# Kernel tuning notes

Measured on AMD Instinct MI355X. Metric: run time of the kernel, lower is better.

Reference implementation:

```python
import jax, jax.numpy as jnp
import numpy as np

STRIDE = 15           # cfg.shm.dilation_kernel
PAD = STRIDE // 2
P = 1048576           # cfg.shm.max_n_pixel (static sparse-pixel budget)


def dilate(alpha):
    # mask = (0.01 < alpha < 0.99); then 15x15 max-pool, stride 1, pad 7 (same size)
    m = jnp.logical_and(alpha > 0.01, alpha < 0.99).astype(alpha.dtype)
    return jax.lax.reduce_window(
        m, -jnp.inf, jax.lax.max,
        (1, 1, STRIDE, STRIDE), (1, 1, 1, 1),
        [(0, 0), (0, 0), (PAD, PAD), (PAD, PAD)])


def setup_inputs() -> dict:
    key = jax.random.key(0)
    ks = jax.random.split(key, 8)
    d = 128
    return {
        'image': jax.random.normal(ks[0], (8, 3, 512, 512), jnp.float32),
        'lr_pred': jax.random.uniform(ks[1], (8, 1, 512, 512), jnp.float32),
        'W1': jax.random.normal(ks[2], (4, d), jnp.float32) * 0.5,
        'b1': jnp.zeros((d,), jnp.float32),
        'W2': jax.random.normal(ks[3], (d, d), jnp.float32) * (1.0 / np.sqrt(d)),
        'b2': jnp.zeros((d,), jnp.float32),
        'W3': jax.random.normal(ks[4], (d, 1), jnp.float32) * (1.0 / np.sqrt(d)),
        'b3': jnp.zeros((1,), jnp.float32),
    }


def reference(image, lr_pred, W1, b1, W2, b2, W3, b3):
    B, C, H, W = image.shape
    mask = dilate(lr_pred)                       # [B,1,H,W] dilated uncertainty mask

    # generate_sparse_inputs: cat(img, (lr_pred-0.5)/0.5) channels-last, gather where mask>0
    feat = jnp.concatenate([image, (lr_pred - 0.5) / 0.5], axis=1)  # [B,4,H,W]
    feat = feat.transpose(0, 2, 3, 1).reshape(-1, C + 1)            # [B*H*W, 4]
    mflat = mask.reshape(-1)                                        # [B*H*W]

    (idx,) = jnp.nonzero(mflat > 0, size=P, fill_value=0)           # static-size gather
    count = jnp.sum(mflat > 0)
    valid = (jnp.arange(P) < count).astype(feat.dtype)              # [P]

    # torch's generate_sparse_inputs runs under no_grad -> stop_gradient on gather
    x = jax.lax.stop_gradient(feat[idx])                            # [P,4]

    # stand-in sparse head (shm): per-pixel MLP with sigmoid alpha output
    h = jax.nn.relu(x @ W1 + b1)
    h = jax.nn.relu(h @ W2 + b2)
    pred = jax.nn.sigmoid(h @ W3 + b3)[:, 0]                        # [P]

    # scatter predictions back to dense grid; ungathered masked pixels keep lr_pred
    scattered = jnp.zeros_like(mflat).at[idx].add(pred * valid)
    covered = jnp.zeros_like(mflat).at[idx].add(valid)
    lrf = lr_pred.reshape(-1)
    dense = scattered + (1.0 - covered) * lrf

    # final blend: pred*mask + lr_pred*(1-mask)
    final = dense * mflat + lrf * (1.0 - mflat)
    return final.reshape(B, 1, H, W)
```

## Files before the change

### kernel.cpp

```cpp
#include <hip/hip_runtime.h>
#include <hip/hip_bf16.h>
#include <math.h>

#define BB 8
#define HH 512
#define WW 512
#define NPIX (BB * HH * WW)
#define HWPIX (HH * WW)
#define PBUD 1048576
#define RAD 7
#define NB (NPIX / 256)
#define NMLP (NPIX / 128)

typedef __attribute__((ext_vector_type(4))) float f32x4;
typedef __attribute__((ext_vector_type(8))) short short8;
typedef __attribute__((ext_vector_type(2))) unsigned int u32x2;
typedef __attribute__((ext_vector_type(4))) unsigned int u32x4;

__device__ __forceinline__ unsigned short f2bf(float f) {
    unsigned int u = __float_as_uint(f);
    unsigned int r = (u + 0x7fffu + ((u >> 16) & 1u)) >> 16;
    return (unsigned short)r;
}

__device__ __forceinline__ unsigned int pkbf(float a, float b) {
    __hip_bfloat162 h = __float22bfloat162_rn(make_float2(a, b));
    return *(unsigned int*)&h;
}

__global__ void k_prep(const float* __restrict__ w2, const float* __restrict__ w1,
                       const float* __restrict__ b1,
                       unsigned short* __restrict__ w2f, unsigned short* __restrict__ w1f) {
    int i = blockIdx.x * 256 + threadIdx.x;
    if (i < 16384) {
        int e  = i & 7;
        int l  = (i >> 3) & 63;
        int ks = (i >> 9) & 3;
        int jc = i >> 11;
        int j = jc * 16 + (l & 15);
        int k = ks * 32 + ((l >> 4) & 3) * 8 + e;
        w2f[i] = f2bf(w2[k * 128 + j]);
    } else {
        int i2 = i - 16384;
        int e  = i2 & 7;
        int l  = (i2 >> 3) & 63;
        int fi = i2 >> 9;
        int j = fi * 16 + (l & 15);
        int k = ((l >> 4) & 3) * 8 + e;
        float v = (k < 4) ? w1[k * 128 + j] : ((k == 4) ? b1[j] : 0.0f);
        w1f[i2] = f2bf(v);
    }
}

__global__ void k_rowdil(const float* __restrict__ lr, unsigned char* __restrict__ rowdil) {
    int p = blockIdx.x * 256 + threadIdx.x;
    int w = p & (WW - 1);
    int row0 = p - w;
    int lo = w - RAD; if (lo < 0) lo = 0;
    int hi = w + RAD; if (hi > WW - 1) hi = WW - 1;
    unsigned char any = 0;
    for (int x = lo; x <= hi; ++x) {
        float v = lr[row0 + x];
        any |= (unsigned char)(v > 0.01f && v < 0.99f);
    }
    rowdil[p] = any;
}

__global__ void k_coldil(const unsigned char* __restrict__ rowdil,
                         unsigned char* __restrict__ dm,
                         unsigned char* __restrict__ rankb,
                         int* __restrict__ gsum) {
    int p = blockIdx.x * 256 + threadIdx.x;
    int h = (p >> 9) & (HH - 1);
    int lo = h - RAD; if (lo < 0) lo = 0;
    int hi = h + RAD; if (hi > HH - 1) hi = HH - 1;
    lo -= h; hi -= h;
    unsigned char any = 0;
    for (int d = lo; d <= hi; ++d) any |= rowdil[p + d * WW];
    dm[p] = any;

    unsigned long long bal = __ballot(any != 0);
    __shared__ int wsum[4];
    int lane = threadIdx.x & 63;
    int wid  = threadIdx.x >> 6;
    if (lane == 0) wsum[wid] = __popcll(bal);
    __syncthreads();
    int pre = __popcll(bal & ((1ull << lane) - 1ull));
    int woff = 0;
    for (int i = 0; i < wid; ++i) woff += wsum[i];
    rankb[p] = (unsigned char)(woff + pre);
    if (threadIdx.x == 0) gsum[blockIdx.x] = wsum[0] + wsum[1] + wsum[2] + wsum[3];
}

__global__ void k_scan(const int* __restrict__ gsum, int* __restrict__ goff) {
    __shared__ int tsum[1024];
    int t = threadIdx.x;
    int base = t * 8;
    int v[8];
    int s = 0;
#pragma unroll
    for (int i = 0; i < 8; ++i) { v[i] = gsum[base + i]; s += v[i]; }
    tsum[t] = s;
    __syncthreads();
    for (int off = 1; off < 1024; off <<= 1) {
        int x = tsum[t];
        int y = (t >= off) ? tsum[t - off] : 0;
        __syncthreads();
        tsum[t] = x + y;
        __syncthreads();
    }
    int run = (t == 0) ? 0 : tsum[t - 1];
#pragma unroll
    for (int i = 0; i < 8; ++i) { goff[base + i] = run; run += v[i]; }
}

__global__ __launch_bounds__(256, 3)
void k_mlp(const float* __restrict__ image, const float* __restrict__ lr,
           const unsigned short* __restrict__ w1f, const unsigned short* __restrict__ w2f,
           const float* __restrict__ b2, const float* __restrict__ w3,
           const float* __restrict__ b3,
           const unsigned char* __restrict__ dm, const unsigned char* __restrict__ rankb,
           const int* __restrict__ goff, float* __restrict__ out) {
    __shared__ __align__(16) char lds[43008];
    __shared__ int s_any;
    int g  = blockIdx.x;
    int p0 = g * 128;
    int t  = threadIdx.x;

    if (t == 0) s_any = 0;
    __syncthreads();
    float lrv0 = 0.f;
    if (t < 128) {
        int p = p0 + t;
        lrv0 = lr[p];
        if (dm[p] && (goff[p >> 8] + (int)rankb[p] < PBUD)) s_any = 1;
    }
    __syncthreads();
    if (!s_any) {
        if (t < 128) out[p0 + t] = lrv0;
        return;
    }

    if (t < 128) {
        int p = p0 + t;
        size_t bimg = (size_t)(p >> 18) * 3 * HWPIX + (p & (HWPIX - 1));
        float x0 = image[bimg];
        float x1 = image[bimg + HWPIX];
        float x2 = image[bimg + 2 * HWPIX];
        float x3 = 2.0f * lrv0 - 1.0f;
        char* xr = lds + 32768 + t * 80;
        u32x4 d0 = { pkbf(x0, x1), pkbf(x2, x3), pkbf(1.0f, 0.0f), 0u };
        u32x4 z  = { 0u, 0u, 0u, 0u };
        *(u32x4*)(xr)      = d0;
        *(u32x4*)(xr + 16) = z;
        *(u32x4*)(xr + 32) = z;
        *(u32x4*)(xr + 48) = z;
        *(u32x4*)(xr + 64) = z;
    }

    int w    = t >> 6;
    int l    = t & 63;
    int lr16 = l & 15;
    int lh   = (l >> 4) & 3;

    const short8* wf1 = (const short8*)w1f;
    short8 a1_0 = wf1[(w * 2 + 0) * 64 + l];
    short8 a1_1 = wf1[(w * 2 + 1) * 64 + l];
    __syncthreads();

#pragma unroll
    for (int jc = 0; jc < 8; ++jc) {
        int px = jc * 16 + lr16;
        short8 xb = *(const short8*)(lds + 32768 + px * 80 + lh * 16);
        f32x4 c0 = {0.f, 0.f, 0.f, 0.f};
        f32x4 c1 = {0.f, 0.f, 0.f, 0.f};
        c0 = __builtin_amdgcn_mfma_f32_16x16x32_bf16(a1_0, xb, c0, 0, 0, 0);
        c1 = __builtin_amdgcn_mfma_f32_16x16x32_bf16(a1_1, xb, c1, 0, 0, 0);
        int swz = (px & 15) << 4;
        {
            int j0 = (w * 2 + 0) * 16 + lh * 4;
            u32x2 u = { pkbf(fmaxf(c0[0], 0.f), fmaxf(c0[1], 0.f)),
                        pkbf(fmaxf(c0[2], 0.f), fmaxf(c0[3], 0.f)) };
            *(u32x2*)(lds + (((px << 8) | (j0 << 1)) ^ swz)) = u;
        }
        {
            int j1 = (w * 2 + 1) * 16 + lh * 4;
            u32x2 u = { pkbf(fmaxf(c1[0], 0.f), fmaxf(c1[1], 0.f)),
                        pkbf(fmaxf(c1[2], 0.f), fmaxf(c1[3], 0.f)) };
            *(u32x2*)(lds + (((px << 8) | (j1 << 1)) ^ swz)) = u;
        }
    }
    __syncthreads();

    int rowbase = w * 32;
    short8 af[2][4];
#pragma unroll
    for (int ks = 0; ks < 4; ++ks) {
#pragma unroll
        for (int mt = 0; mt < 2; ++mt) {
            int row = rowbase + mt * 16 + lr16;
            int a = (((row << 8) | (ks << 6) | (lh << 4))) ^ ((row & 15) << 4);
            af[mt][ks] = *(const short8*)(lds + a);
        }
    }

    float b2v[8], w3v[8];
#pragma unroll
    for (int jc = 0; jc < 8; ++jc) {
        int col = jc * 16 + lr16;
        b2v[jc] = b2[col];
        w3v[jc] = w3[col];
    }
    float b3v = b3[0];

    f32x4 acc[2][8];
#pragma unroll
    for (int mt = 0; mt < 2; ++mt)
#pragma unroll
        for (int jc = 0; jc < 8; ++jc)
            acc[mt][jc] = (f32x4){b2v[jc], b2v[jc], b2v[jc], b2v[jc]};

    const short8* wf = (const short8*)w2f;
#pragma unroll
    for (int jc = 0; jc < 8; ++jc) {
        short8 bf[4];
#pragma unroll
        for (int ks = 0; ks < 4; ++ks) bf[ks] = wf[(jc * 4 + ks) * 64 + l];
#pragma unroll
        for (int ks = 0; ks < 4; ++ks) {
            acc[0][jc] = __builtin_amdgcn_mfma_f32_16x16x32_bf16(af[0][ks], bf[ks], acc[0][jc], 0, 0, 0);
            acc[1][jc] = __builtin_amdgcn_mfma_f32_16x16x32_bf16(af[1][ks], bf[ks], acc[1][jc], 0, 0, 0);
        }
    }

#pragma unroll
    for (int mt = 0; mt < 2; ++mt) {
#pragma unroll
        for (int r = 0; r < 4; ++r) {
            int row = rowbase + mt * 16 + lh * 4 + r;
            float part = 0.f;
#pragma unroll
            for (int jc = 0; jc < 8; ++jc)
                part += fmaxf(acc[mt][jc][r], 0.f) * w3v[jc];
            part += __shfl_xor(part, 1);
            part += __shfl_xor(part, 2);
            part += __shfl_xor(part, 4);
            part += __shfl_xor(part, 8);
            if (lr16 == 0) {
                int p = p0 + row;
                float lrv = lr[p];
                bool s = dm[p] && (goff[p >> 8] + (int)rankb[p] < PBUD);
                float logit = b3v + part;
                out[p] = s ? (1.0f / (1.0f + __expf(-logit))) : lrv;
            }
        }
    }
}

extern "C" void kernel_launch(void* const* d_in, const int* in_sizes, int n_in,
                              void* d_out, int out_size, void* d_ws, size_t ws_size,
                              hipStream_t stream) {
    const float* image = (const float*)d_in[0];
    const float* lr    = (const float*)d_in[1];
    const float* w1    = (const float*)d_in[2];
    const float* b1    = (const float*)d_in[3];
    const float* w2    = (const float*)d_in[4];
    const float* b2    = (const float*)d_in[5];
    const float* w3    = (const float*)d_in[6];
    const float* b3    = (const float*)d_in[7];
    float* out = (float*)d_out;

    char* ws = (char*)d_ws;
    unsigned char* rowdil = (unsigned char*)ws;
    unsigned char* dm     = (unsigned char*)(ws + (size_t)NPIX);
    unsigned char* rankb  = (unsigned char*)(ws + 2 * (size_t)NPIX);
    int* gsum             = (int*)(ws + 3 * (size_t)NPIX);
    int* goff             = (int*)(ws + 3 * (size_t)NPIX + NB * 4);
    unsigned short* w2f   = (unsigned short*)(ws + 3 * (size_t)NPIX + 2 * NB * 4);
    unsigned short* w1f   = w2f + 16384;

    k_prep  <<<80, 256, 0, stream>>>(w2, w1, b1, w2f, w1f);
    k_rowdil<<<NPIX / 256, 256, 0, stream>>>(lr, rowdil);
    k_coldil<<<NB, 256, 0, stream>>>(rowdil, dm, rankb, gsum);
    k_scan  <<<1, 1024, 0, stream>>>(gsum, goff);
    k_mlp   <<<NMLP, 256, 0, stream>>>(image, lr, w1f, w2f, b2, w3, b3,
                                       dm, rankb, goff, out);
}
```

Before: 152.3 us.

## Split MLP work over 8 waves by output column with LDS reduction

The MLP kernel moves from 4 waves, each owning 32 pixel rows and all 128 hidden columns, to 8 waves, each owning 16 hidden columns across all 128 pixels. Each wave keeps only its slice of W2 in registers and streams activation fragments from LDS, and per-wave partial logits are reduced through LDS before the sigmoid. The input staging shrinks to 16 bytes per pixel plus a shared zero row, and the early-exit test uses a wave ballot instead of a shared flag. The aim is to cut register pressure and raise occupancy. The cost is more LDS reads (activations are re-read by every wave) and an extra barrier for the final reduction.

```diff
diff --git a/kernel.cpp b/kernel.cpp
--- a/kernel.cpp
+++ b/kernel.cpp
@@ -11,6 +11,11 @@
 #define RAD 7
 #define NB (NPIX / 256)
 #define NMLP (NPIX / 128)
+
+#define XOFF  32768
+#define ZROW  (XOFF + 2048)
+#define FLAG0 (XOFF + 2080)
+#define PART  XOFF
 
 typedef __attribute__((ext_vector_type(4))) float f32x4;
 typedef __attribute__((ext_vector_type(8))) short short8;
@@ -114,146 +119,106 @@
     for (int i = 0; i < 8; ++i) { goff[base + i] = run; run += v[i]; }
 }
 
-__global__ __launch_bounds__(256, 3)
+__global__ __launch_bounds__(512, 6)
 void k_mlp(const float* __restrict__ image, const float* __restrict__ lr,
            const unsigned short* __restrict__ w1f, const unsigned short* __restrict__ w2f,
            const float* __restrict__ b2, const float* __restrict__ w3,
            const float* __restrict__ b3,
            const unsigned char* __restrict__ dm, const unsigned char* __restrict__ rankb,
            const int* __restrict__ goff, float* __restrict__ out) {
-    __shared__ __align__(16) char lds[43008];
-    __shared__ int s_any;
-    int g  = blockIdx.x;
-    int p0 = g * 128;
+    __shared__ __align__(16) char lds[36864];
+    int p0 = blockIdx.x * 128;
     int t  = threadIdx.x;
-
-    if (t == 0) s_any = 0;
-    __syncthreads();
-    float lrv0 = 0.f;
+    int w  = t >> 6;
+    int l  = t & 63;
+    int lr16 = l & 15;
+    int lh   = (l >> 4) & 3;
+
+    const short8* wf1 = (const short8*)w1f;
+    short8 a1 = wf1[w * 64 + l];
+    float b2v = b2[w * 16 + lr16];
+    float w3v = w3[w * 16 + lr16];
+    float b3v = b3[0];
+
+    bool  sel = false;
+    float lrv = 0.f;
     if (t < 128) {
         int p = p0 + t;
-        lrv0 = lr[p];
-        if (dm[p] && (goff[p >> 8] + (int)rankb[p] < PBUD)) s_any = 1;
-    }
-    __syncthreads();
-    if (!s_any) {
-        if (t < 128) out[p0 + t] = lrv0;
-        return;
-    }
-
-    if (t < 128) {
-        int p = p0 + t;
+        lrv = lr[p];
+        sel = dm[p] && (goff[p >> 8] + (int)rankb[p] < PBUD);
         size_t bimg = (size_t)(p >> 18) * 3 * HWPIX + (p & (HWPIX - 1));
         float x0 = image[bimg];
         float x1 = image[bimg + HWPIX];
         float x2 = image[bimg + 2 * HWPIX];
-        float x3 = 2.0f * lrv0 - 1.0f;
-        char* xr = lds + 32768 + t * 80;
+        float x3 = 2.0f * lrv - 1.0f;
         u32x4 d0 = { pkbf(x0, x1), pkbf(x2, x3), pkbf(1.0f, 0.0f), 0u };
-        u32x4 z  = { 0u, 0u, 0u, 0u };
-        *(u32x4*)(xr)      = d0;
-        *(u32x4*)(xr + 16) = z;
-        *(u32x4*)(xr + 32) = z;
-        *(u32x4*)(xr + 48) = z;
-        *(u32x4*)(xr + 64) = z;
-    }
-
-    int w    = t >> 6;
-    int l    = t & 63;
-    int lr16 = l & 15;
-    int lh   = (l >> 4) & 3;
-
-    const short8* wf1 = (const short8*)w1f;
-    short8 a1_0 = wf1[(w * 2 + 0) * 64 + l];
-    short8 a1_1 = wf1[(w * 2 + 1) * 64 + l];
-    __syncthreads();
+        *(u32x4*)(lds + XOFF + t * 16) = d0;
+    }
+    if (t == 128) *(u32x4*)(lds + ZROW) = (u32x4){0u, 0u, 0u, 0u};
+    if (t < 128) {
+        unsigned long long bal = __ballot(sel);
+        if (l == 0) *(int*)(lds + FLAG0 + w * 4) = (bal != 0ull) ? 1 : 0;
+    }
+    __syncthreads();
+    int any = *(const int*)(lds + FLAG0) | *(const int*)(lds + FLAG0 + 4);
+    if (!any) {
+        if (t < 128) out[p0 + t] = lrv;
+        return;
+    }
 
 #pragma unroll
     for (int jc = 0; jc < 8; ++jc) {
         int px = jc * 16 + lr16;
-        short8 xb = *(const short8*)(lds + 32768 + px * 80 + lh * 16);
-        f32x4 c0 = {0.f, 0.f, 0.f, 0.f};
-        f32x4 c1 = {0.f, 0.f, 0.f, 0.f};
-        c0 = __builtin_amdgcn_mfma_f32_16x16x32_bf16(a1_0, xb, c0, 0, 0, 0);
-        c1 = __builtin_amdgcn_mfma_f32_16x16x32_bf16(a1_1, xb, c1, 0, 0, 0);
-        int swz = (px & 15) << 4;
-        {
-            int j0 = (w * 2 + 0) * 16 + lh * 4;
-            u32x2 u = { pkbf(fmaxf(c0[0], 0.f), fmaxf(c0[1], 0.f)),
-                        pkbf(fmaxf(c0[2], 0.f), fmaxf(c0[3], 0.f)) };
-            *(u32x2*)(lds + (((px << 8) | (j0 << 1)) ^ swz)) = u;
+        const char* xaddr = (lh == 0) ? (lds + XOFF + px * 16) : (lds + ZROW);
+        short8 xb = *(const short8*)xaddr;
+        f32x4 c = {0.f, 0.f, 0.f, 0.f};
+        c = __builtin_amdgcn_mfma_f32_16x16x32_bf16(a1, xb, c, 0, 0, 0);
+        int j0 = w * 16 + lh * 4;
+        u32x2 u = { pkbf(fmaxf(c[0], 0.f), fmaxf(c[1], 0.f)),
+                    pkbf(fmaxf(c[2], 0.f), fmaxf(c[3], 0.f)) };
+        *(u32x2*)(lds + (((px << 8) | (j0 << 1)) ^ (lr16 << 4))) = u;
+    }
+
+    const short8* wf2 = (const short8*)w2f;
+    short8 bf[4];
+#pragma unroll
+    for (int ks = 0; ks < 4; ++ks) bf[ks] = wf2[(w * 4 + ks) * 64 + l];
+    __syncthreads();
+
+    f32x4 acc[8];
+#pragma unroll
+    for (int mt = 0; mt < 8; ++mt) acc[mt] = (f32x4){b2v, b2v, b2v, b2v};
+#pragma unroll
+    for (int mt = 0; mt < 8; ++mt) {
+#pragma unroll
+        for (int ks = 0; ks < 4; ++ks) {
+            int row = mt * 16 + lr16;
+            short8 af = *(const short8*)(lds + ((((row << 8) | (ks << 6) | (lh << 4))) ^ (lr16 << 4)));
+            acc[mt] = __builtin_amdgcn_mfma_f32_16x16x32_bf16(af, bf[ks], acc[mt], 0, 0, 0);
         }
-        {
-            int j1 = (w * 2 + 1) * 16 + lh * 4;
-            u32x2 u = { pkbf(fmaxf(c1[0], 0.f), fmaxf(c1[1], 0.f)),
-                        pkbf(fmaxf(c1[2], 0.f), fmaxf(c1[3], 0.f)) };
-            *(u32x2*)(lds + (((px << 8) | (j1 << 1)) ^ swz)) = u;
-        }
-    }
-    __syncthreads();
-
-    int rowbase = w * 32;
-    short8 af[2][4];
-#pragma unroll
-    for (int ks = 0; ks < 4; ++ks) {
-#pragma unroll
-        for (int mt = 0; mt < 2; ++mt) {
-            int row = rowbase + mt * 16 + lr16;
-            int a = (((row << 8) | (ks << 6) | (lh << 4))) ^ ((row & 15) << 4);
-            af[mt][ks] = *(const short8*)(lds + a);
-        }
-    }
-
-    float b2v[8], w3v[8];
-#pragma unroll
-    for (int jc = 0; jc < 8; ++jc) {
-        int col = jc * 16 + lr16;
-        b2v[jc] = b2[col];
-        w3v[jc] = w3[col];
-    }
-    float b3v = b3[0];
-
-    f32x4 acc[2][8];
-#pragma unroll
-    for (int mt = 0; mt < 2; ++mt)
-#pragma unroll
-        for (int jc = 0; jc < 8; ++jc)
-            acc[mt][jc] = (f32x4){b2v[jc], b2v[jc], b2v[jc], b2v[jc]};
-
-    const short8* wf = (const short8*)w2f;
-#pragma unroll
-    for (int jc = 0; jc < 8; ++jc) {
-        short8 bf[4];
-#pragma unroll
-        for (int ks = 0; ks < 4; ++ks) bf[ks] = wf[(jc * 4 + ks) * 64 + l];
-#pragma unroll
-        for (int ks = 0; ks < 4; ++ks) {
-            acc[0][jc] = __builtin_amdgcn_mfma_f32_16x16x32_bf16(af[0][ks], bf[ks], acc[0][jc], 0, 0, 0);
-            acc[1][jc] = __builtin_amdgcn_mfma_f32_16x16x32_bf16(af[1][ks], bf[ks], acc[1][jc], 0, 0, 0);
-        }
-    }
-
-#pragma unroll
-    for (int mt = 0; mt < 2; ++mt) {
+    }
+
+#pragma unroll
+    for (int mt = 0; mt < 8; ++mt) {
 #pragma unroll
         for (int r = 0; r < 4; ++r) {
-            int row = rowbase + mt * 16 + lh * 4 + r;
-            float part = 0.f;
-#pragma unroll
-            for (int jc = 0; jc < 8; ++jc)
-                part += fmaxf(acc[mt][jc][r], 0.f) * w3v[jc];
+            float part = fmaxf(acc[mt][r], 0.f) * w3v;
             part += __shfl_xor(part, 1);
             part += __shfl_xor(part, 2);
             part += __shfl_xor(part, 4);
             part += __shfl_xor(part, 8);
             if (lr16 == 0) {
-                int p = p0 + row;
-                float lrv = lr[p];
-                bool s = dm[p] && (goff[p >> 8] + (int)rankb[p] < PBUD);
-                float logit = b3v + part;
-                out[p] = s ? (1.0f / (1.0f + __expf(-logit))) : lrv;
+                int px = mt * 16 + lh * 4 + r;
+                *(float*)(lds + PART + w * 512 + px * 4) = part;
             }
         }
+    }
+    __syncthreads();
+    if (t < 128) {
+        float s = b3v;
+#pragma unroll
+        for (int ww = 0; ww < 8; ++ww) s += *(const float*)(lds + PART + ww * 512 + t * 4);
+        out[p0 + t] = sel ? (1.0f / (1.0f + __expf(-s))) : lrv;
     }
 }
 
@@ -283,6 +248,6 @@
     k_rowdil<<<NPIX / 256, 256, 0, stream>>>(lr, rowdil);
     k_coldil<<<NB, 256, 0, stream>>>(rowdil, dm, rankb, gsum);
     k_scan  <<<1, 1024, 0, stream>>>(gsum, goff);
-    k_mlp   <<<NMLP, 256, 0, stream>>>(image, lr, w1f, w2f, b2, w3, b3,
+    k_mlp   <<<NMLP, 512, 0, stream>>>(image, lr, w1f, w2f, b2, w3, b3,
                                        dm, rankb, goff, out);
 }
```

Result: slower. 186.6 us (+22.5%).

## Compact MLP layer-1 staging, drop barriers, and raise occupancy to four blocks

Applied to the files above, without the earlier changes.

The input staging rows shrink from 80 to 16 bytes, with a shared zero row serving the padded K lanes. The any-selected check becomes a wavefront ballot written to LDS flags, which removes one barrier. Layer 1 is reorganised so each wave computes all 128 hidden units for its own 32 pixels, so the barrier between layer 1 and layer 2 is gone. LDS use falls and launch bounds go from 3 to 4 blocks per CU. This adds register pressure, since all eight W1 fragments are now held per thread, and it relies on each wave reading back only the rows it wrote itself.

```diff
diff --git a/kernel.cpp b/kernel.cpp
--- a/kernel.cpp
+++ b/kernel.cpp
@@ -11,6 +11,10 @@
 #define RAD 7
 #define NB (NPIX / 256)
 #define NMLP (NPIX / 128)
+
+#define XOFF  32768
+#define ZROW  (XOFF + 2048)
+#define FLAGS (XOFF + 2064)
 
 typedef __attribute__((ext_vector_type(4))) float f32x4;
 typedef __attribute__((ext_vector_type(8))) short short8;
@@ -114,85 +118,68 @@
     for (int i = 0; i < 8; ++i) { goff[base + i] = run; run += v[i]; }
 }
 
-__global__ __launch_bounds__(256, 3)
+__global__ __launch_bounds__(256, 4)
 void k_mlp(const float* __restrict__ image, const float* __restrict__ lr,
            const unsigned short* __restrict__ w1f, const unsigned short* __restrict__ w2f,
            const float* __restrict__ b2, const float* __restrict__ w3,
            const float* __restrict__ b3,
            const unsigned char* __restrict__ dm, const unsigned char* __restrict__ rankb,
            const int* __restrict__ goff, float* __restrict__ out) {
-    __shared__ __align__(16) char lds[43008];
-    __shared__ int s_any;
-    int g  = blockIdx.x;
-    int p0 = g * 128;
+    __shared__ __align__(16) char lds[34944];
+    int p0 = blockIdx.x * 128;
     int t  = threadIdx.x;
-
-    if (t == 0) s_any = 0;
-    __syncthreads();
-    float lrv0 = 0.f;
+    int w    = t >> 6;
+    int l    = t & 63;
+    int lr16 = l & 15;
+    int lh   = l >> 4;
+
+    const short8* wf1 = (const short8*)w1f;
+    short8 a1[8];
+#pragma unroll
+    for (int jt = 0; jt < 8; ++jt) a1[jt] = wf1[jt * 64 + l];
+
+    bool  sel = false;
+    float lrv = 0.f;
     if (t < 128) {
         int p = p0 + t;
-        lrv0 = lr[p];
-        if (dm[p] && (goff[p >> 8] + (int)rankb[p] < PBUD)) s_any = 1;
-    }
-    __syncthreads();
-    if (!s_any) {
-        if (t < 128) out[p0 + t] = lrv0;
-        return;
-    }
-
-    if (t < 128) {
-        int p = p0 + t;
+        lrv = lr[p];
+        sel = dm[p] && (goff[p >> 8] + (int)rankb[p] < PBUD);
         size_t bimg = (size_t)(p >> 18) * 3 * HWPIX + (p & (HWPIX - 1));
         float x0 = image[bimg];
         float x1 = image[bimg + HWPIX];
         float x2 = image[bimg + 2 * HWPIX];
-        float x3 = 2.0f * lrv0 - 1.0f;
-        char* xr = lds + 32768 + t * 80;
+        float x3 = 2.0f * lrv - 1.0f;
         u32x4 d0 = { pkbf(x0, x1), pkbf(x2, x3), pkbf(1.0f, 0.0f), 0u };
-        u32x4 z  = { 0u, 0u, 0u, 0u };
-        *(u32x4*)(xr)      = d0;
-        *(u32x4*)(xr + 16) = z;
-        *(u32x4*)(xr + 32) = z;
-        *(u32x4*)(xr + 48) = z;
-        *(u32x4*)(xr + 64) = z;
-    }
-
-    int w    = t >> 6;
-    int l    = t & 63;
-    int lr16 = l & 15;
-    int lh   = (l >> 4) & 3;
-
-    const short8* wf1 = (const short8*)w1f;
-    short8 a1_0 = wf1[(w * 2 + 0) * 64 + l];
-    short8 a1_1 = wf1[(w * 2 + 1) * 64 + l];
+        *(u32x4*)(lds + XOFF + t * 16) = d0;
+        unsigned long long bal = __ballot(sel);
+        if (l == 0) *(int*)(lds + FLAGS + w * 4) = (bal != 0ull) ? 1 : 0;
+    }
+    if (t == 128) *(u32x4*)(lds + ZROW) = (u32x4){0u, 0u, 0u, 0u};
     __syncthreads();
-
-#pragma unroll
-    for (int jc = 0; jc < 8; ++jc) {
-        int px = jc * 16 + lr16;
-        short8 xb = *(const short8*)(lds + 32768 + px * 80 + lh * 16);
-        f32x4 c0 = {0.f, 0.f, 0.f, 0.f};
-        f32x4 c1 = {0.f, 0.f, 0.f, 0.f};
-        c0 = __builtin_amdgcn_mfma_f32_16x16x32_bf16(a1_0, xb, c0, 0, 0, 0);
-        c1 = __builtin_amdgcn_mfma_f32_16x16x32_bf16(a1_1, xb, c1, 0, 0, 0);
-        int swz = (px & 15) << 4;
-        {
-            int j0 = (w * 2 + 0) * 16 + lh * 4;
-            u32x2 u = { pkbf(fmaxf(c0[0], 0.f), fmaxf(c0[1], 0.f)),
-                        pkbf(fmaxf(c0[2], 0.f), fmaxf(c0[3], 0.f)) };
-            *(u32x2*)(lds + (((px << 8) | (j0 << 1)) ^ swz)) = u;
-        }
-        {
-            int j1 = (w * 2 + 1) * 16 + lh * 4;
-            u32x2 u = { pkbf(fmaxf(c1[0], 0.f), fmaxf(c1[1], 0.f)),
-                        pkbf(fmaxf(c1[2], 0.f), fmaxf(c1[3], 0.f)) };
-            *(u32x2*)(lds + (((px << 8) | (j1 << 1)) ^ swz)) = u;
-        }
-    }
-    __syncthreads();
-
-    int rowbase = w * 32;
+    int any = *(const int*)(lds + FLAGS) | *(const int*)(lds + FLAGS + 4);
+    if (!any) {
+        if (t < 128) out[p0 + t] = lrv;
+        return;
+    }
+
+    int pxb = w * 32;
+#pragma unroll
+    for (int pxt = 0; pxt < 2; ++pxt) {
+        int px = pxb + pxt * 16 + lr16;
+        const char* xaddr = (lh == 0) ? (lds + XOFF + px * 16) : (lds + ZROW);
+        short8 xb = *(const short8*)xaddr;
+#pragma unroll
+        for (int jt = 0; jt < 8; ++jt) {
+            f32x4 c = {0.f, 0.f, 0.f, 0.f};
+            c = __builtin_amdgcn_mfma_f32_16x16x32_bf16(a1[jt], xb, c, 0, 0, 0);
+            int j0 = jt * 16 + lh * 4;
+            u32x2 u = { pkbf(fmaxf(c[0], 0.f), fmaxf(c[1], 0.f)),
+                        pkbf(fmaxf(c[2], 0.f), fmaxf(c[3], 0.f)) };
+            *(u32x2*)(lds + (((px << 8) | (j0 << 1)) ^ ((px & 15) << 4))) = u;
+        }
+    }
+
+    int rowbase = pxb;
     short8 af[2][4];
 #pragma unroll
     for (int ks = 0; ks < 4; ++ks) {
@@ -248,10 +235,10 @@
             part += __shfl_xor(part, 8);
             if (lr16 == 0) {
                 int p = p0 + row;
-                float lrv = lr[p];
+                float lrvp = lr[p];
                 bool s = dm[p] && (goff[p >> 8] + (int)rankb[p] < PBUD);
                 float logit = b3v + part;
-                out[p] = s ? (1.0f / (1.0f + __expf(-logit))) : lrv;
+                out[p] = s ? (1.0f / (1.0f + __expf(-logit))) : lrvp;
             }
         }
     }
```

Measured after the change: 140.2 us. 1.09x faster.
